# Optimization experiments

Measured on AMD Instinct MI355X. Metric: run time of the kernel, lower is better.

## Reference

```python
import jax, jax.numpy as jnp
import numpy as np

T, B, D = 2048, 16, 1024


def setup_inputs() -> dict:
    key = jax.random.key(0)
    ks = jax.random.split(key, 8)
    std = 1.0 / D ** 0.5
    x = jax.random.normal(ks[0], (T, B, D), dtype=jnp.float32)
    h0 = jnp.zeros((B, D), dtype=jnp.float32)
    Wx = jax.random.uniform(ks[1], (D, D), jnp.float32, -std, std)
    R = jax.random.uniform(ks[2], (D, D), jnp.float32, -std, std)
    bias = jnp.zeros((D,), dtype=jnp.float32)
    W_delta = jax.random.uniform(ks[3], (D, D), jnp.float32, -std * 0.1, std * 0.1)
    b_delta = jnp.full((D,), 3.0, dtype=jnp.float32)  # delta_init
    A = jax.random.uniform(ks[4], (D,), jnp.float32, -0.5, 0.5)  # A_init_range
    W_gate_x = jax.random.uniform(ks[5], (D, D), jnp.float32, -std, std)
    W_gate_h = jax.random.uniform(ks[6], (D, D), jnp.float32, -std, std)
    b_gate = jnp.zeros((D,), dtype=jnp.float32)
    return {"x": x, "h0": h0, "Wx": Wx, "R": R, "bias": bias,
            "W_delta": W_delta, "b_delta": b_delta, "A": A,
            "W_gate_x": W_gate_x, "W_gate_h": W_gate_h, "b_gate": b_gate}


def reference(x, h0, Wx, R, bias, W_delta, b_delta, A, W_gate_x, W_gate_h, b_gate):
    # Input-dependent timestep: dt = softplus(x @ W_delta^T + b_delta), [T,B,D]
    dt = jax.nn.softplus(jnp.einsum('tbd,ed->tbe', x, W_delta) + b_delta)
    # Mamba-style log parameterization: decay_rate in (0,1), alpha in (0,1)
    decay_rate = jnp.exp(-jnp.exp(A))                 # [D]
    alpha = jnp.exp(-dt * decay_rate)                 # [T,B,D]
    # Precompute input projection once (big GEMM outside the scan)
    wx = jnp.einsum('tbd,ed->tbe', x, Wx) + bias      # [T,B,D]

    def step(h, inp):
        wx_t, a_t = inp                               # [B,D], [B,D]
        cand = jnp.tanh(h @ R.T + wx_t)               # nonlinear candidate
        h_new = a_t * h + (1.0 - a_t) * cand          # exponential blend
        return h_new, h_new

    _, h_out = jax.lax.scan(step, h0, (wx, alpha))    # h_out: [T,B,D] == h[1:]

    # h+x selective output gate
    gate_raw = (jnp.einsum('tbd,ed->tbe', x, W_gate_x)
                + jnp.einsum('tbd,ed->tbe', h_out, W_gate_h) + b_gate)
    return h_out * jax.nn.silu(gate_raw)
```

## Files before the change

kernel.cpp:

```cpp
#include <hip/hip_runtime.h>
#include <cstdint>
#include <cstddef>

typedef _Float16 f16;
typedef _Float16 f16x8 __attribute__((ext_vector_type(8)));
typedef _Float16 f16x4v __attribute__((ext_vector_type(4)));
typedef float f32x4 __attribute__((ext_vector_type(4)));
typedef unsigned uint2v __attribute__((ext_vector_type(2)));

#define TT 2048
#define BB 16
#define DD 1024
#define MM (TT*BB)
#define LDST 40
#define FPAD 16

__global__ void cvt_kernel(const float* __restrict__ in, f16* __restrict__ out, int n4){
  int stride = gridDim.x * blockDim.x;
  for (int j = blockIdx.x*blockDim.x + threadIdx.x; j < n4; j += stride){
    float4 v = ((const float4*)in)[j];
    f16x4v o;
    o[0]=(f16)v.x; o[1]=(f16)v.y; o[2]=(f16)v.z; o[3]=(f16)v.w;
    ((f16x4v*)out)[j] = o;
  }
}

__global__ void cvt5_kernel(const float* __restrict__ a0, const float* __restrict__ a1,
                            const float* __restrict__ a2, const float* __restrict__ a3,
                            const float* __restrict__ a4,
                            f16* __restrict__ o0, f16* __restrict__ o1,
                            f16* __restrict__ o2, f16* __restrict__ o3, f16* __restrict__ o4){
  const float* src[5] = {a0,a1,a2,a3,a4};
  f16* dst[5] = {o0,o1,o2,o3,o4};
  int which = blockIdx.y;
  const float* in = src[which];
  f16* out = dst[which];
  int j = blockIdx.x*blockDim.x + threadIdx.x;
  float4 v = ((const float4*)in)[j];
  f16x4v o;
  o[0]=(f16)v.x; o[1]=(f16)v.y; o[2]=(f16)v.z; o[3]=(f16)v.w;
  ((f16x4v*)out)[j] = o;
}

__global__ void init_rec_kernel(const float* __restrict__ h0, f16* __restrict__ hbuf,
                                unsigned* __restrict__ flags){
  int tid = blockIdx.x*blockDim.x + threadIdx.x;
  if (tid < 64*FPAD) flags[tid] = 0u;
  if (tid < BB*DD) hbuf[tid] = (f16)h0[tid];
}

__global__ __launch_bounds__(256)
void gemm_f16_kernel(const f16* __restrict__ A, const f16* __restrict__ Bw,
                     float* __restrict__ out32, f16* __restrict__ out16,
                     const float* __restrict__ vec1, const float* __restrict__ vec2,
                     const f16* __restrict__ gxin, int epi)
{
  __shared__ f16 As[128*LDST];
  __shared__ f16 Bs[128*LDST];
  const int K = DD;
  int tid = threadIdx.x;
  int l = tid & 63, w = tid >> 6;
  int wr = w >> 1, wc = w & 1;
  int bm = blockIdx.x, bn = blockIdx.y;

  f32x4 acc[4][4];
  #pragma unroll
  for (int i=0;i<4;++i)
    #pragma unroll
    for (int j=0;j<4;++j)
      acc[i][j] = (f32x4){0.f,0.f,0.f,0.f};

  const int r0 = tid >> 2;
  const int q  = tid & 3;

  for (int kt = 0; kt < K/32; ++kt){
    __syncthreads();
    #pragma unroll
    for (int hh=0; hh<2; ++hh){
      int row = hh*64 + r0;
      uint4 va = *(const uint4*)(A  + (size_t)(bm*128+row)*K + kt*32 + q*8);
      uint4 vb = *(const uint4*)(Bw + (size_t)(bn*128+row)*K + kt*32 + q*8);
      *(uint4*)(As + row*LDST + q*8) = va;
      *(uint4*)(Bs + row*LDST + q*8) = vb;
    }
    __syncthreads();
    int lr = l & 15, kg = (l >> 4) * 8;
    f16x8 af[4], bf[4];
    #pragma unroll
    for (int i=0;i<4;++i){
      af[i] = *(const f16x8*)(As + (wr*64 + i*16 + lr)*LDST + kg);
      bf[i] = *(const f16x8*)(Bs + (wc*64 + i*16 + lr)*LDST + kg);
    }
    #pragma unroll
    for (int i=0;i<4;++i)
      #pragma unroll
      for (int j=0;j<4;++j)
        acc[i][j] = __builtin_amdgcn_mfma_f32_16x16x32_f16(af[i], bf[j], acc[i][j], 0,0,0);
  }

  int lr = l & 15, lh = l >> 4;
  #pragma unroll
  for (int i=0;i<4;++i){
    #pragma unroll
    for (int j=0;j<4;++j){
      #pragma unroll
      for (int r=0;r<4;++r){
        int row = bm*128 + wr*64 + i*16 + lh*4 + r;
        int col = bn*128 + wc*64 + j*16 + lr;
        float v = acc[i][j][r];
        size_t off = (size_t)row*DD + col;
        if (epi == 0){
          out16[off] = (f16)(v + vec1[col]);
        } else if (epi == 1){
          float pre = v + vec1[col];
          float sp  = (pre > 20.f) ? pre : log1pf(expf(pre));
          float decay = expf(-expf(vec2[col]));
          out16[off] = (f16)expf(-sp*decay);
        } else if (epi == 2){
          out16[off] = (f16)(v + vec1[col]);
        } else {
          float g = v + (float)gxin[off];
          float hval = (float)A[off];
          out32[off] = hval * g / (1.f + expf(-g));
        }
      }
    }
  }
}

__global__ __launch_bounds__(64)
void rec_kernel(const f16* __restrict__ Rf, const f16* __restrict__ wx,
                const f16* __restrict__ alpha, const float* __restrict__ h0,
                f16* __restrict__ hbuf, f16* __restrict__ hout,
                unsigned* __restrict__ flags)
{
  __shared__ f16 Rlds[32*64*8];

  int l = threadIdx.x;
  int j = blockIdx.x;
  int e0 = j * 16;

  #pragma unroll
  for (int kt=0; kt<32; ++kt){
    int e = e0 + (l & 15);
    int d = kt*32 + (l >> 4)*8;
    *(uint4*)(Rlds + ((size_t)kt*64 + l)*8) = *(const uint4*)(Rf + (size_t)e*DD + d);
  }

  int b = l & 15, rr0 = (l >> 4) * 4;
  float4 hstate = *(const float4*)(h0 + (size_t)b*DD + e0 + rr0);
  __syncthreads();

  f32x4 wxv, alv;
  {
    f16x4v wh = *(const f16x4v*)(wx + (size_t)b*DD + e0 + rr0);
    f16x4v ah = *(const f16x4v*)(alpha + (size_t)b*DD + e0 + rr0);
    #pragma unroll
    for (int r=0;r<4;++r){ wxv[r] = (float)wh[r]; alv[r] = (float)ah[r]; }
  }

  for (int t = 0; t < TT; ++t){
    if (t > 0){
      const unsigned* fp = flags + l*FPAD;
      int guard = 0;
      unsigned long long notready = 1ull;
      while (notready && guard < 2000000){
        unsigned fv = __hip_atomic_load(fp, __ATOMIC_RELAXED, __HIP_MEMORY_SCOPE_AGENT);
        notready = __ballot(fv < (unsigned)t);
        ++guard;
        if (notready) __builtin_amdgcn_s_sleep(1);
      }
    }

    const f16* hb = hbuf + (size_t)(t & 1) * (BB*DD);
    f16x8 hfr[32];
    #pragma unroll
    for (int kt=0; kt<32; ++kt){
      const f16* hp = hb + (size_t)b*DD + kt*32 + (l >> 4)*8;
      asm volatile("global_load_dwordx4 %0, %1, off sc0 sc1"
                   : "=v"(hfr[kt]) : "v"(hp) : "memory");
    }

    f32x4 accv[4];
    #pragma unroll
    for (int c=0;c<4;++c) accv[c] = (f32x4){0.f,0.f,0.f,0.f};

    asm volatile("s_waitcnt vmcnt(16)" ::: "memory");
    __builtin_amdgcn_sched_barrier(0);
    #pragma unroll
    for (int kt=0; kt<16; ++kt){
      f16x8 a = *(const f16x8*)(Rlds + ((size_t)kt*64 + l)*8);
      accv[kt&3] = __builtin_amdgcn_mfma_f32_16x16x32_f16(a, hfr[kt], accv[kt&3], 0, 0, 0);
    }
    asm volatile("s_waitcnt vmcnt(0)" ::: "memory");
    __builtin_amdgcn_sched_barrier(0);

    int tn = (t+1 < TT) ? (t+1) : t;
    size_t offn = ((size_t)tn*BB + b)*DD + e0 + rr0;
    f16x4v whn = *(const f16x4v*)(wx + offn);
    f16x4v ahn = *(const f16x4v*)(alpha + offn);

    #pragma unroll
    for (int kt=16; kt<32; ++kt){
      f16x8 a = *(const f16x8*)(Rlds + ((size_t)kt*64 + l)*8);
      accv[kt&3] = __builtin_amdgcn_mfma_f32_16x16x32_f16(a, hfr[kt], accv[kt&3], 0, 0, 0);
    }
    f32x4 acc = (accv[0]+accv[1]) + (accv[2]+accv[3]);

    f16x4v h4;
    float hs[4] = {hstate.x, hstate.y, hstate.z, hstate.w};
    #pragma unroll
    for (int r=0;r<4;++r){
      float z = acc[r] + wxv[r];
      float cand = tanhf(z);
      float hn = alv[r]*hs[r] + (1.f - alv[r])*cand;
      hs[r] = hn;
      h4[r] = (f16)hn;
    }
    hstate = (float4){hs[0], hs[1], hs[2], hs[3]};

    f16* hw = hbuf + (size_t)((t+1) & 1) * (BB*DD) + (size_t)b*DD + e0 + rr0;
    uint2v hv = __builtin_bit_cast(uint2v, h4);
    asm volatile("global_store_dwordx2 %0, %1, off sc0 sc1"
                 :: "v"(hw), "v"(hv) : "memory");
    asm volatile("s_waitcnt vmcnt(0)" ::: "memory");
    if (l == 0)
      __hip_atomic_store(flags + j*FPAD, (unsigned)(t+1),
                         __ATOMIC_RELAXED, __HIP_MEMORY_SCOPE_AGENT);

    *(f16x4v*)(hout + ((size_t)t*BB + b)*DD + e0 + rr0) = h4;
    #pragma unroll
    for (int r=0;r<4;++r){ wxv[r] = (float)whn[r]; alv[r] = (float)ahn[r]; }
  }
}

extern "C" void kernel_launch(void* const* d_in, const int* in_sizes, int n_in,
                              void* d_out, int out_size, void* d_ws, size_t ws_size,
                              hipStream_t stream)
{
  const float* x    = (const float*)d_in[0];
  const float* h0   = (const float*)d_in[1];
  const float* Wx   = (const float*)d_in[2];
  const float* R    = (const float*)d_in[3];
  const float* bias = (const float*)d_in[4];
  const float* Wd   = (const float*)d_in[5];
  const float* bd   = (const float*)d_in[6];
  const float* Aar  = (const float*)d_in[7];
  const float* Wgx  = (const float*)d_in[8];
  const float* Wgh  = (const float*)d_in[9];
  const float* bg   = (const float*)d_in[10];
  float* out = (float*)d_out;

  char* ws = (char*)d_ws;
  size_t off = 0;
  auto carve = [&](size_t bytes) -> void* {
    void* p = ws + off;
    off += (bytes + 255) & ~(size_t)255;
    return p;
  };
  f16* x16    = (f16*)carve((size_t)MM*DD*2);
  f16* Wx16   = (f16*)carve((size_t)DD*DD*2);
  f16* Wd16   = (f16*)carve((size_t)DD*DD*2);
  f16* Wgx16  = (f16*)carve((size_t)DD*DD*2);
  f16* Wgh16  = (f16*)carve((size_t)DD*DD*2);
  f16* R16    = (f16*)carve((size_t)DD*DD*2);
  f16* wx16   = (f16*)carve((size_t)MM*DD*2);
  f16* al16   = (f16*)carve((size_t)MM*DD*2);
  f16* gx16   = (f16*)carve((size_t)MM*DD*2);
  f16* hout16 = (f16*)carve((size_t)MM*DD*2);
  f16* hbuf   = (f16*)carve((size_t)2*BB*DD*2);
  unsigned* flags = (unsigned*)carve(64*FPAD*4);
  if (off > ws_size) return;

  cvt_kernel<<<1024, 256, 0, stream>>>(x, x16, MM*DD/4);
  dim3 g5(DD*DD/4/256, 5);
  cvt5_kernel<<<g5, 256, 0, stream>>>(Wx, Wd, Wgx, Wgh, R,
                                      Wx16, Wd16, Wgx16, Wgh16, R16);
  init_rec_kernel<<<64, 256, 0, stream>>>(h0, hbuf, flags);

  dim3 gg(MM/128, DD/128);
  gemm_f16_kernel<<<gg, 256, 0, stream>>>(x16, Wx16,  nullptr, wx16, bias, nullptr, nullptr, 0);
  gemm_f16_kernel<<<gg, 256, 0, stream>>>(x16, Wd16,  nullptr, al16, bd,   Aar,     nullptr, 1);
  gemm_f16_kernel<<<gg, 256, 0, stream>>>(x16, Wgx16, nullptr, gx16, bg,   nullptr, nullptr, 2);

  rec_kernel<<<64, 64, 0, stream>>>(R16, wx16, al16, h0, hbuf, hout16, flags);

  gemm_f16_kernel<<<gg, 256, 0, stream>>>(hout16, Wgh16, out, nullptr, nullptr, nullptr, gx16, 3);
}
```

Before: 7.280 ms.

## Fuse input GEMMs into one launch, fold gate-x GEMM into final, finer rec waits

The wx and alpha projections now run as a single launch with a doubled grid that picks its weight matrix by block column. The gate-x projection is no longer written to an intermediate buffer; the final kernel accumulates both x@Wgx and h@Wgh in one K loop of length 2D. This removes a full f16 MxD write and read plus launch overhead. The recurrent kernel's wait on the h-fragment loads is split into four stages, so MFMAs start sooner after each quarter of the loads arrives, which targets the serial critical path.

```diff
diff --git a/kernel.cpp b/kernel.cpp
--- a/kernel.cpp
+++ b/kernel.cpp
@@ -49,80 +49,102 @@
   if (tid < BB*DD) hbuf[tid] = (f16)h0[tid];
 }
 
+#define GEMM_PROLOGUE() \
+  __shared__ f16 As[128*LDST]; \
+  __shared__ f16 Bs[128*LDST]; \
+  int tid = threadIdx.x; \
+  int l = tid & 63, w = tid >> 6; \
+  int wr = w >> 1, wc = w & 1; \
+  f32x4 acc[4][4]; \
+  _Pragma("unroll") for (int i=0;i<4;++i) _Pragma("unroll") for (int jj=0;jj<4;++jj) \
+    acc[i][jj] = (f32x4){0.f,0.f,0.f,0.f}; \
+  const int r0 = tid >> 2; \
+  const int q  = tid & 3;
+
+#define GEMM_KSTEP(Asrc, Bsrc, ktl) { \
+  __syncthreads(); \
+  _Pragma("unroll") for (int hh=0; hh<2; ++hh){ \
+    int row = hh*64 + r0; \
+    uint4 va = *(const uint4*)((Asrc) + (size_t)(bm*128+row)*DD + (ktl)*32 + q*8); \
+    uint4 vb = *(const uint4*)((Bsrc) + (size_t)(bcol*128+row)*DD + (ktl)*32 + q*8); \
+    *(uint4*)(As + row*LDST + q*8) = va; \
+    *(uint4*)(Bs + row*LDST + q*8) = vb; \
+  } \
+  __syncthreads(); \
+  int lr = l & 15, kg = (l >> 4) * 8; \
+  f16x8 af[4], bf[4]; \
+  _Pragma("unroll") for (int i=0;i<4;++i){ \
+    af[i] = *(const f16x8*)(As + (wr*64 + i*16 + lr)*LDST + kg); \
+    bf[i] = *(const f16x8*)(Bs + (wc*64 + i*16 + lr)*LDST + kg); \
+  } \
+  _Pragma("unroll") for (int i=0;i<4;++i) \
+    _Pragma("unroll") for (int jj=0;jj<4;++jj) \
+      acc[i][jj] = __builtin_amdgcn_mfma_f32_16x16x32_f16(af[i], bf[jj], acc[i][jj], 0,0,0); \
+}
+
 __global__ __launch_bounds__(256)
-void gemm_f16_kernel(const f16* __restrict__ A, const f16* __restrict__ Bw,
-                     float* __restrict__ out32, f16* __restrict__ out16,
-                     const float* __restrict__ vec1, const float* __restrict__ vec2,
-                     const f16* __restrict__ gxin, int epi)
+void gemm_wa_kernel(const f16* __restrict__ x16,
+                    const f16* __restrict__ Wx16, const f16* __restrict__ Wd16,
+                    f16* __restrict__ wxo, f16* __restrict__ alo,
+                    const float* __restrict__ bias, const float* __restrict__ bd,
+                    const float* __restrict__ Aar)
 {
-  __shared__ f16 As[128*LDST];
-  __shared__ f16 Bs[128*LDST];
-  const int K = DD;
-  int tid = threadIdx.x;
-  int l = tid & 63, w = tid >> 6;
-  int wr = w >> 1, wc = w & 1;
   int bm = blockIdx.x, bn = blockIdx.y;
-
-  f32x4 acc[4][4];
-  #pragma unroll
-  for (int i=0;i<4;++i)
-    #pragma unroll
-    for (int j=0;j<4;++j)
-      acc[i][j] = (f32x4){0.f,0.f,0.f,0.f};
-
-  const int r0 = tid >> 2;
-  const int q  = tid & 3;
-
-  for (int kt = 0; kt < K/32; ++kt){
-    __syncthreads();
-    #pragma unroll
-    for (int hh=0; hh<2; ++hh){
-      int row = hh*64 + r0;
-      uint4 va = *(const uint4*)(A  + (size_t)(bm*128+row)*K + kt*32 + q*8);
-      uint4 vb = *(const uint4*)(Bw + (size_t)(bn*128+row)*K + kt*32 + q*8);
-      *(uint4*)(As + row*LDST + q*8) = va;
-      *(uint4*)(Bs + row*LDST + q*8) = vb;
-    }
-    __syncthreads();
-    int lr = l & 15, kg = (l >> 4) * 8;
-    f16x8 af[4], bf[4];
-    #pragma unroll
-    for (int i=0;i<4;++i){
-      af[i] = *(const f16x8*)(As + (wr*64 + i*16 + lr)*LDST + kg);
-      bf[i] = *(const f16x8*)(Bs + (wc*64 + i*16 + lr)*LDST + kg);
-    }
-    #pragma unroll
-    for (int i=0;i<4;++i)
-      #pragma unroll
-      for (int j=0;j<4;++j)
-        acc[i][j] = __builtin_amdgcn_mfma_f32_16x16x32_f16(af[i], bf[j], acc[i][j], 0,0,0);
-  }
+  int alpha_path = (bn >= 8);
+  int bcol = bn & 7;
+  const f16* Bw = alpha_path ? Wd16 : Wx16;
+
+  GEMM_PROLOGUE();
+  for (int kt = 0; kt < 32; ++kt) GEMM_KSTEP(x16, Bw, kt);
 
   int lr = l & 15, lh = l >> 4;
   #pragma unroll
   for (int i=0;i<4;++i){
     #pragma unroll
-    for (int j=0;j<4;++j){
+    for (int jj=0;jj<4;++jj){
       #pragma unroll
       for (int r=0;r<4;++r){
         int row = bm*128 + wr*64 + i*16 + lh*4 + r;
-        int col = bn*128 + wc*64 + j*16 + lr;
-        float v = acc[i][j][r];
+        int col = bcol*128 + wc*64 + jj*16 + lr;
+        float v = acc[i][jj][r];
         size_t off = (size_t)row*DD + col;
-        if (epi == 0){
-          out16[off] = (f16)(v + vec1[col]);
-        } else if (epi == 1){
-          float pre = v + vec1[col];
+        if (!alpha_path){
+          wxo[off] = (f16)(v + bias[col]);
+        } else {
+          float pre = v + bd[col];
           float sp  = (pre > 20.f) ? pre : log1pf(expf(pre));
-          float decay = expf(-expf(vec2[col]));
-          out16[off] = (f16)expf(-sp*decay);
-        } else if (epi == 2){
-          out16[off] = (f16)(v + vec1[col]);
-        } else {
-          float g = v + (float)gxin[off];
-          float hval = (float)A[off];
-          out32[off] = hval * g / (1.f + expf(-g));
+          float decay = expf(-expf(Aar[col]));
+          alo[off] = (f16)expf(-sp*decay);
         }
+      }
+    }
+  }
+}
+
+__global__ __launch_bounds__(256)
+void gemm_fin_kernel(const f16* __restrict__ hout16, const f16* __restrict__ x16,
+                     const f16* __restrict__ Wgh16, const f16* __restrict__ Wgx16,
+                     float* __restrict__ out, const float* __restrict__ bg)
+{
+  int bm = blockIdx.x, bcol = blockIdx.y;
+
+  GEMM_PROLOGUE();
+  for (int kt = 0; kt < 32; ++kt) GEMM_KSTEP(hout16, Wgh16, kt);
+  for (int kt = 0; kt < 32; ++kt) GEMM_KSTEP(x16,    Wgx16, kt);
+
+  int lr = l & 15, lh = l >> 4;
+  #pragma unroll
+  for (int i=0;i<4;++i){
+    #pragma unroll
+    for (int jj=0;jj<4;++jj){
+      #pragma unroll
+      for (int r=0;r<4;++r){
+        int row = bm*128 + wr*64 + i*16 + lh*4 + r;
+        int col = bcol*128 + wc*64 + jj*16 + lr;
+        float g = acc[i][jj][r] + bg[col];
+        size_t off = (size_t)row*DD + col;
+        float hval = (float)hout16[off];
+        out[off] = hval * g / (1.f + expf(-g));
       }
     }
   }
@@ -185,14 +207,21 @@
     #pragma unroll
     for (int c=0;c<4;++c) accv[c] = (f32x4){0.f,0.f,0.f,0.f};
 
+    asm volatile("s_waitcnt vmcnt(24)" ::: "memory");
+    __builtin_amdgcn_sched_barrier(0);
+    #pragma unroll
+    for (int kt=0; kt<8; ++kt){
+      f16x8 a = *(const f16x8*)(Rlds + ((size_t)kt*64 + l)*8);
+      accv[kt&3] = __builtin_amdgcn_mfma_f32_16x16x32_f16(a, hfr[kt], accv[kt&3], 0, 0, 0);
+    }
     asm volatile("s_waitcnt vmcnt(16)" ::: "memory");
     __builtin_amdgcn_sched_barrier(0);
     #pragma unroll
-    for (int kt=0; kt<16; ++kt){
+    for (int kt=8; kt<16; ++kt){
       f16x8 a = *(const f16x8*)(Rlds + ((size_t)kt*64 + l)*8);
       accv[kt&3] = __builtin_amdgcn_mfma_f32_16x16x32_f16(a, hfr[kt], accv[kt&3], 0, 0, 0);
     }
-    asm volatile("s_waitcnt vmcnt(0)" ::: "memory");
+    asm volatile("s_waitcnt vmcnt(8)" ::: "memory");
     __builtin_amdgcn_sched_barrier(0);
 
     int tn = (t+1 < TT) ? (t+1) : t;
@@ -201,7 +230,14 @@
     f16x4v ahn = *(const f16x4v*)(alpha + offn);
 
     #pragma unroll
-    for (int kt=16; kt<32; ++kt){
+    for (int kt=16; kt<24; ++kt){
+      f16x8 a = *(const f16x8*)(Rlds + ((size_t)kt*64 + l)*8);
+      accv[kt&3] = __builtin_amdgcn_mfma_f32_16x16x32_f16(a, hfr[kt], accv[kt&3], 0, 0, 0);
+    }
+    asm volatile("s_waitcnt vmcnt(0)" ::: "memory");
+    __builtin_amdgcn_sched_barrier(0);
+    #pragma unroll
+    for (int kt=24; kt<32; ++kt){
       f16x8 a = *(const f16x8*)(Rlds + ((size_t)kt*64 + l)*8);
       accv[kt&3] = __builtin_amdgcn_mfma_f32_16x16x32_f16(a, hfr[kt], accv[kt&3], 0, 0, 0);
     }
@@ -266,7 +302,6 @@
   f16* R16    = (f16*)carve((size_t)DD*DD*2);
   f16* wx16   = (f16*)carve((size_t)MM*DD*2);
   f16* al16   = (f16*)carve((size_t)MM*DD*2);
-  f16* gx16   = (f16*)carve((size_t)MM*DD*2);
   f16* hout16 = (f16*)carve((size_t)MM*DD*2);
   f16* hbuf   = (f16*)carve((size_t)2*BB*DD*2);
   unsigned* flags = (unsigned*)carve(64*FPAD*4);
@@ -278,12 +313,11 @@
                                       Wx16, Wd16, Wgx16, Wgh16, R16);
   init_rec_kernel<<<64, 256, 0, stream>>>(h0, hbuf, flags);
 
-  dim3 gg(MM/128, DD/128);
-  gemm_f16_kernel<<<gg, 256, 0, stream>>>(x16, Wx16,  nullptr, wx16, bias, nullptr, nullptr, 0);
-  gemm_f16_kernel<<<gg, 256, 0, stream>>>(x16, Wd16,  nullptr, al16, bd,   Aar,     nullptr, 1);
-  gemm_f16_kernel<<<gg, 256, 0, stream>>>(x16, Wgx16, nullptr, gx16, bg,   nullptr, nullptr, 2);
+  dim3 gwa(MM/128, 16);
+  gemm_wa_kernel<<<gwa, 256, 0, stream>>>(x16, Wx16, Wd16, wx16, al16, bias, bd, Aar);
 
   rec_kernel<<<64, 64, 0, stream>>>(R16, wx16, al16, h0, hbuf, hout16, flags);
 
-  gemm_f16_kernel<<<gg, 256, 0, stream>>>(hout16, Wgh16, out, nullptr, nullptr, nullptr, gx16, 3);
-}
+  dim3 gfin(MM/128, DD/128);
+  gemm_fin_kernel<<<gfin, 256, 0, stream>>>(hout16, x16, Wgh16, Wgx16, out, bg);
+}
```

After: 7.092 ms. -2.6%, faster.
